# Kernel optimization log

Measured on AMD Instinct MI355X. Metric: run time of the kernel, lower is better.

Reference implementation:

```python
import jax, jax.numpy as jnp
import numpy as np
import math

D_MODEL, N_HEADS, SHARP = 1024, 16, 2.0
D_HEAD = D_MODEL // N_HEADS
B, S = 2, 2048


def setup_inputs() -> dict:
    key = jax.random.key(0)
    ks = jax.random.split(key, 12)
    s = 0.02
    d, h = D_MODEL, D_MODEL // 2
    return {
        'x': jax.random.normal(ks[0], (B, S, d), jnp.float32),
        'mask': jnp.ones((B, S), jnp.int32),
        'Wq': jax.random.normal(ks[1], (d, d), jnp.float32) * s,
        'bq': jnp.zeros((d,), jnp.float32),
        'Wk': jax.random.normal(ks[2], (d, d), jnp.float32) * s,
        'bk': jnp.zeros((d,), jnp.float32),
        'Wv': jax.random.normal(ks[3], (d, d), jnp.float32) * s,
        'bv': jnp.zeros((d,), jnp.float32),
        'Wo': jax.random.normal(ks[4], (d, d), jnp.float32) * s,
        'bo': jnp.zeros((d,), jnp.float32),
        'Wm1': jax.random.normal(ks[5], (h, d), jnp.float32) * s,
        'bm1': jnp.zeros((h,), jnp.float32),
        'Wm2': jax.random.normal(ks[6], (1, h), jnp.float32) * s,
        'bm2': jnp.zeros((1,), jnp.float32),
    }


def reference(x, mask, Wq, bq, Wk, bk, Wv, bv, Wo, bo, Wm1, bm1, Wm2, bm2):
    Bsz, Ssz, _ = x.shape
    lin = lambda t, W, b: jnp.einsum('bsd,ed->bse', t, W) + b  # torch Linear: x @ W.T + b
    split = lambda t: t.reshape(Bsz, Ssz, N_HEADS, D_HEAD).transpose(0, 2, 1, 3)  # [B,H,S,Dh]
    q, k, v = split(lin(x, Wq, bq)), split(lin(x, Wk, bk)), split(lin(x, Wv, bv))
    scores = jnp.einsum('bhqd,bhkd->bhqk', q, k) / math.sqrt(D_HEAD)  # [B,H,S,S]
    scores = jnp.where(mask[:, None, None, :] == 0, -jnp.inf, scores)
    # mechanism MLP: Linear -> GELU(exact) -> Linear -> [B,S]
    hmid = jax.nn.gelu(lin(x, Wm1, bm1), approximate=False)
    mech_logits = lin(hmid, Wm2, bm2).squeeze(-1)
    mech_strengths = jax.nn.softmax(mech_logits, axis=-1)  # [B,S]
    scores = scores + SHARP * mech_strengths[:, None, None, :]
    attn = jax.nn.softmax(scores, axis=-1)
    ctx = jnp.einsum('bhqk,bhkd->bhqd', attn, v)
    ctx = ctx.transpose(0, 2, 1, 3).reshape(Bsz, Ssz, D_MODEL)
    out = jnp.einsum('bsd,ed->bse', ctx, Wo) + bo
    return (out, mech_strengths)
```

## Files before the change

kernel.cpp:

```cpp
#include <hip/hip_runtime.h>
#include <hip/hip_fp16.h>
#include <math.h>

typedef _Float16 half4_t __attribute__((ext_vector_type(4)));
typedef _Float16 half8_t __attribute__((ext_vector_type(8)));
typedef float float4_t __attribute__((ext_vector_type(4)));

static constexpr int DMODEL = 1024;
static constexpr int SLEN   = 2048;
static constexpr int NHEADS = 16;
static constexpr int MTOT   = 4096;


__global__ __launch_bounds__(256) void pack_all_kernel(
    const float* __restrict__ x,
    const float* __restrict__ Wq, const float* __restrict__ Wk,
    const float* __restrict__ Wv, const float* __restrict__ Wo,
    const float* __restrict__ Wm1,
    _Float16* __restrict__ xP, _Float16* __restrict__ wqP,
    _Float16* __restrict__ wkP, _Float16* __restrict__ wvP,
    _Float16* __restrict__ woP, _Float16* __restrict__ wm1P) {
  int bx = blockIdx.x;
  const float* src; _Float16* dst; int lb;
  if (blockIdx.y == 0) {
    if (bx >= 2048) return;
    src = x; dst = xP; lb = bx;
  } else {
    if (bx < 512)       { src = Wq;  dst = wqP;  lb = bx; }
    else if (bx < 1024) { src = Wk;  dst = wkP;  lb = bx - 512; }
    else if (bx < 1536) { src = Wv;  dst = wvP;  lb = bx - 1024; }
    else if (bx < 2048) { src = Wo;  dst = woP;  lb = bx - 1536; }
    else                { src = Wm1; dst = wm1P; lb = bx - 2048; }
  }
  int c = lb * 256 + threadIdx.x;
  int lane = c & 63;
  int ks = (c >> 6) & 31;
  int rt = c >> 11;
  int row = 16 * rt + (lane & 15);
  int col = 32 * ks + 8 * (lane >> 4);
  const float* sp = src + (size_t)row * 1024 + col;
  float4_t v0 = *(const float4_t*)sp;
  float4_t v1 = *(const float4_t*)(sp + 4);
  half8_t h;
  h[0] = (_Float16)v0[0]; h[1] = (_Float16)v0[1];
  h[2] = (_Float16)v0[2]; h[3] = (_Float16)v0[3];
  h[4] = (_Float16)v1[0]; h[5] = (_Float16)v1[1];
  h[6] = (_Float16)v1[2]; h[7] = (_Float16)v1[3];
  *(half8_t*)(dst + (size_t)c * 8) = h;
}

__global__ __launch_bounds__(256, 2) void proj_kernel(
    const _Float16* __restrict__ xP,
    const _Float16* __restrict__ wqP, const _Float16* __restrict__ wkP,
    const _Float16* __restrict__ wvP, const _Float16* __restrict__ wm1P,
    const float* __restrict__ bq, const float* __restrict__ bk,
    const float* __restrict__ bv, const float* __restrict__ bm1,
    _Float16* __restrict__ Qh, _Float16* __restrict__ Kh,
    _Float16* __restrict__ Vh, _Float16* __restrict__ Hm) {
  int z = blockIdx.z;
  const _Float16* W; const float* bias; _Float16* out; int N; bool act = false;
  if (z == 0)      { W = wqP;  bias = bq;  out = Qh; N = 1024; }
  else if (z == 1) { W = wkP;  bias = bk;  out = Kh; N = 1024; }
  else if (z == 2) { W = wvP;  bias = bv;  out = Vh; N = 1024; }
  else             { W = wm1P; bias = bm1; out = Hm; N = 512; act = true; }
  int colB = blockIdx.y * 128;
  if (colB >= N) return;
  int wave = threadIdx.x >> 6, lane = threadIdx.x & 63;
  int lr = lane & 15, lg = lane >> 4;
  int row0 = blockIdx.x * 128 + (wave >> 1) * 64;
  int col0 = colB + (wave & 1) * 64;
  int rt0 = row0 >> 4, ct0 = col0 >> 4;
  float4_t acc[4][4];
#pragma unroll
  for (int i = 0; i < 4; i++)
#pragma unroll
    for (int j = 0; j < 4; j++) acc[i][j] = (float4_t){0.f, 0.f, 0.f, 0.f};
  for (int ks = 0; ks < 32; ks++) {
    half8_t af[4], bf[4];
#pragma unroll
    for (int i = 0; i < 4; i++)
      af[i] = *(const half8_t*)(xP + (((size_t)(rt0 + i) * 32 + ks) << 9) + (lane << 3));
#pragma unroll
    for (int j = 0; j < 4; j++)
      bf[j] = *(const half8_t*)(W + (((size_t)(ct0 + j) * 32 + ks) << 9) + (lane << 3));
#pragma unroll
    for (int i = 0; i < 4; i++)
#pragma unroll
      for (int j = 0; j < 4; j++)
        acc[i][j] = __builtin_amdgcn_mfma_f32_16x16x32_f16(af[i], bf[j], acc[i][j], 0, 0, 0);
  }
#pragma unroll
  for (int j = 0; j < 4; j++) {
    int col = col0 + 16 * j + lr;
    float bb = bias[col];
#pragma unroll
    for (int i = 0; i < 4; i++) {
#pragma unroll
      for (int r = 0; r < 4; r++) {
        int row = row0 + 16 * i + 4 * lg + r;
        float v = acc[i][j][r] + bb;
        if (act) v = 0.5f * v * (1.0f + erff(v * 0.70710678118f));
        out[(size_t)row * N + col] = (_Float16)v;
      }
    }
  }
}

__global__ __launch_bounds__(256, 2) void outproj_kernel(
    const _Float16* __restrict__ ctxh, const _Float16* __restrict__ woP,
    const float* __restrict__ bo, float* __restrict__ out) {
  int wave = threadIdx.x >> 6, lane = threadIdx.x & 63;
  int lr = lane & 15, lg = lane >> 4;
  int row0 = blockIdx.x * 128 + (wave >> 1) * 64;
  int col0 = blockIdx.y * 128 + (wave & 1) * 64;
  int ct0 = col0 >> 4;
  const _Float16* Ap = ctxh + (size_t)(row0 + lr) * 1024 + 8 * lg;
  float4_t acc[4][4];
#pragma unroll
  for (int i = 0; i < 4; i++)
#pragma unroll
    for (int j = 0; j < 4; j++) acc[i][j] = (float4_t){0.f, 0.f, 0.f, 0.f};
  for (int ks = 0; ks < 32; ks++) {
    half8_t af[4], bf[4];
#pragma unroll
    for (int i = 0; i < 4; i++)
      af[i] = *(const half8_t*)(Ap + (size_t)(16 * i) * 1024 + 32 * ks);
#pragma unroll
    for (int j = 0; j < 4; j++)
      bf[j] = *(const half8_t*)(woP + (((size_t)(ct0 + j) * 32 + ks) << 9) + (lane << 3));
#pragma unroll
    for (int i = 0; i < 4; i++)
#pragma unroll
      for (int j = 0; j < 4; j++)
        acc[i][j] = __builtin_amdgcn_mfma_f32_16x16x32_f16(af[i], bf[j], acc[i][j], 0, 0, 0);
  }
#pragma unroll
  for (int j = 0; j < 4; j++) {
    int col = col0 + 16 * j + lr;
    float bb = bo[col];
#pragma unroll
    for (int i = 0; i < 4; i++) {
#pragma unroll
      for (int r = 0; r < 4; r++) {
        int row = row0 + 16 * i + 4 * lg + r;
        out[(size_t)row * 1024 + col] = acc[i][j][r] + bb;
      }
    }
  }
}

__global__ __launch_bounds__(256) void mech_logits_kernel(
    const _Float16* __restrict__ Hm, const float* __restrict__ Wm2,
    const float* __restrict__ bm2, float* __restrict__ logits) {
  int wave = threadIdx.x >> 6, lane = threadIdx.x & 63;
  int row = blockIdx.x * 4 + wave;
  half8_t hv = *(const half8_t*)(Hm + (size_t)row * 512 + lane * 8);
  float4_t w0 = *(const float4_t*)(Wm2 + lane * 8);
  float4_t w1 = *(const float4_t*)(Wm2 + lane * 8 + 4);
  float s = 0.f;
#pragma unroll
  for (int j = 0; j < 4; j++) s += (float)hv[j] * w0[j];
#pragma unroll
  for (int j = 0; j < 4; j++) s += (float)hv[4 + j] * w1[j];
#pragma unroll
  for (int m = 32; m >= 1; m >>= 1) s += __shfl_xor(s, m, 64);
  if (lane == 0) logits[row] = s + bm2[0];
}

__global__ __launch_bounds__(256) void mech_softmax_kernel(
    const float* __restrict__ logits, float* __restrict__ mech_ws,
    float* __restrict__ mech_out) {
  int b = blockIdx.x;
  int t = threadIdx.x;
  int wave = t >> 6, lane = t & 63;
  __shared__ float redmax[4];
  __shared__ float redsum[4];
  const float4_t* L4 = (const float4_t*)(logits + (size_t)b * 2048);
  float4_t v0 = L4[2 * t], v1 = L4[2 * t + 1];
  float mx = fmaxf(fmaxf(fmaxf(v0[0], v0[1]), fmaxf(v0[2], v0[3])),
                   fmaxf(fmaxf(v1[0], v1[1]), fmaxf(v1[2], v1[3])));
#pragma unroll
  for (int m = 32; m >= 1; m >>= 1) mx = fmaxf(mx, __shfl_xor(mx, m, 64));
  if (lane == 0) redmax[wave] = mx;
  __syncthreads();
  mx = fmaxf(fmaxf(redmax[0], redmax[1]), fmaxf(redmax[2], redmax[3]));
  float e[8];
  float s = 0.f;
#pragma unroll
  for (int j = 0; j < 4; j++) { e[j] = __expf(v0[j] - mx); s += e[j]; }
#pragma unroll
  for (int j = 0; j < 4; j++) { e[4 + j] = __expf(v1[j] - mx); s += e[4 + j]; }
#pragma unroll
  for (int m = 32; m >= 1; m >>= 1) s += __shfl_xor(s, m, 64);
  if (lane == 0) redsum[wave] = s;
  __syncthreads();
  s = redsum[0] + redsum[1] + redsum[2] + redsum[3];
  float inv = 1.0f / s;
  size_t base = (size_t)b * 2048 + (size_t)t * 8;
#pragma unroll
  for (int j = 0; j < 8; j++) {
    float val = e[j] * inv;
    mech_ws[base + j] = val;
    mech_out[base + j] = val;
  }
}

__global__ __launch_bounds__(256) void kpack_kernel(const _Float16* __restrict__ Kh,
                                                    _Float16* __restrict__ KP) {
  int c = blockIdx.x * 256 + threadIdx.x;
  int lane = c & 63;
  int c2 = (c >> 6) & 1;
  int kt = (c >> 7) & 127;
  int bh = c >> 14;
  int b = bh >> 4, h = bh & 15;
  int lr = lane & 15, lg = lane >> 4;
  const _Float16* sp = Kh + (size_t)(b * 2048 + 16 * kt + lr) * 1024 + h * 64 + 32 * c2 + 8 * lg;
  *(half8_t*)(KP + (size_t)c * 8) = *(const half8_t*)sp;
}

__global__ __launch_bounds__(256) void vpack_kernel(const _Float16* __restrict__ Vh,
                                                    _Float16* __restrict__ VP) {
  int bh = blockIdx.y;
  int b = bh >> 4, h = bh & 15;
  int k0 = blockIdx.x * 64;
  __shared__ _Float16 tile[64][68];
  int t = threadIdx.x;
#pragma unroll
  for (int rep = 0; rep < 16; rep++) {
    int idx = rep * 256 + t;
    int k = idx >> 6, d = idx & 63;
    tile[d][k] = Vh[(size_t)(b * 2048 + k0 + k) * 1024 + h * 64 + d];
  }
  __syncthreads();
  _Float16* outb = VP + (((size_t)bh * 128 + (k0 >> 4)) << 10);
#pragma unroll
  for (int rep = 0; rep < 4; rep++) {
    int o4 = rep * 256 + t;
    int lane = o4 & 63;
    int dd = (o4 >> 6) & 3;
    int ktp = o4 >> 8;
    int d = 16 * dd + (lane & 15);
    int k = 16 * ktp + 4 * (lane >> 4);
    half4_t v = *(const half4_t*)&tile[d][k];
    *(half4_t*)(outb + (size_t)o4 * 4) = v;
  }
}

__global__ __launch_bounds__(256, 2) void attn_kernel(
    const _Float16* __restrict__ Qh, const _Float16* __restrict__ KP,
    const _Float16* __restrict__ VP, const float* __restrict__ mech,
    const int* __restrict__ mask, _Float16* __restrict__ ctxh) {
  __shared__ float bias_s[2048];
  int bh = blockIdx.y;
  int b = bh >> 4, h = bh & 15;
  for (int i = threadIdx.x; i < 2048; i += 256)
    bias_s[i] = 2.0f * mech[(size_t)b * 2048 + i] +
                (mask[(size_t)b * 2048 + i] != 0 ? 0.0f : -1e30f);
  __syncthreads();
  int wave = threadIdx.x >> 6, lane = threadIdx.x & 63;
  int lr = lane & 15, lg = lane >> 4;
  int q0 = blockIdx.x * 128 + wave * 32;

  const _Float16* Qbase = Qh + (size_t)(b * 2048 + q0 + lr) * 1024 + h * 64 + 8 * lg;
  half8_t qf[2][2];
  qf[0][0] = *(const half8_t*)(Qbase);
  qf[0][1] = *(const half8_t*)(Qbase + 32);
  qf[1][0] = *(const half8_t*)(Qbase + (size_t)16 * 1024);
  qf[1][1] = *(const half8_t*)(Qbase + (size_t)16 * 1024 + 32);
  const _Float16* KPbh = KP + ((size_t)bh << 17);
  const _Float16* VPbh = VP + ((size_t)bh << 17);

  float m0 = -1e30f, m1 = -1e30f;
  float l0 = 0.0f, l1 = 0.0f;
  float4_t cacc[2][4];
#pragma unroll
  for (int g = 0; g < 2; g++)
#pragma unroll
    for (int dd = 0; dd < 4; dd++) cacc[g][dd] = (float4_t){0.f, 0.f, 0.f, 0.f};

  for (int k0 = 0; k0 < 2048; k0 += 64) {
    int kt0 = k0 >> 4;
    half8_t kf[4][2];
#pragma unroll
    for (int t = 0; t < 4; t++) {
      kf[t][0] = *(const half8_t*)(KPbh + (((size_t)(kt0 + t) * 2 + 0) << 9) + (lane << 3));
      kf[t][1] = *(const half8_t*)(KPbh + (((size_t)(kt0 + t) * 2 + 1) << 9) + (lane << 3));
    }
    half4_t vf[4][4];
#pragma unroll
    for (int dd = 0; dd < 4; dd++)
#pragma unroll
      for (int t = 0; t < 4; t++)
        vf[dd][t] = *(const half4_t*)(VPbh + (((size_t)(kt0 + t) * 4 + dd) << 8) + (lane << 2));
    float4_t bias4[4];
#pragma unroll
    for (int t = 0; t < 4; t++)
      bias4[t] = *(const float4_t*)&bias_s[k0 + 16 * t + 4 * lg];
    float4_t s0[4], s1[4];
#pragma unroll
    for (int t = 0; t < 4; t++) {
      float4_t z = (float4_t){0.f, 0.f, 0.f, 0.f};
      z = __builtin_amdgcn_mfma_f32_16x16x32_f16(kf[t][0], qf[0][0], z, 0, 0, 0);
      z = __builtin_amdgcn_mfma_f32_16x16x32_f16(kf[t][1], qf[0][1], z, 0, 0, 0);
      s0[t] = z;
      float4_t w = (float4_t){0.f, 0.f, 0.f, 0.f};
      w = __builtin_amdgcn_mfma_f32_16x16x32_f16(kf[t][0], qf[1][0], w, 0, 0, 0);
      w = __builtin_amdgcn_mfma_f32_16x16x32_f16(kf[t][1], qf[1][1], w, 0, 0, 0);
      s1[t] = w;
    }
#pragma unroll
    for (int t = 0; t < 4; t++)
#pragma unroll
      for (int r = 0; r < 4; r++) {
        s0[t][r] = s0[t][r] * 0.125f + bias4[t][r];
        s1[t][r] = s1[t][r] * 0.125f + bias4[t][r];
      }
    float tm0 = s0[0][0], tm1 = s1[0][0];
#pragma unroll
    for (int t = 0; t < 4; t++)
#pragma unroll
      for (int r = 0; r < 4; r++) {
        tm0 = fmaxf(tm0, s0[t][r]);
        tm1 = fmaxf(tm1, s1[t][r]);
      }
    tm0 = fmaxf(tm0, __shfl_xor(tm0, 16, 64));
    tm0 = fmaxf(tm0, __shfl_xor(tm0, 32, 64));
    tm1 = fmaxf(tm1, __shfl_xor(tm1, 16, 64));
    tm1 = fmaxf(tm1, __shfl_xor(tm1, 32, 64));
    if (__any((tm0 > m0 + 8.0f) || (tm1 > m1 + 8.0f))) {
      float mn0 = fmaxf(m0, tm0), mn1 = fmaxf(m1, tm1);
      float a0 = __expf(m0 - mn0), a1 = __expf(m1 - mn1);
      l0 *= a0; l1 *= a1;
      m0 = mn0; m1 = mn1;
      int rbase = 4 * lg;
#pragma unroll
      for (int r = 0; r < 4; r++) {
        float b0 = __shfl(a0, rbase + r, 64);
        float b1 = __shfl(a1, rbase + r, 64);
#pragma unroll
        for (int dd = 0; dd < 4; dd++) {
          cacc[0][dd][r] *= b0;
          cacc[1][dd][r] *= b1;
        }
      }
    }
    half4_t pa0[4], pa1[4];
#pragma unroll
    for (int t = 0; t < 4; t++) {
#pragma unroll
      for (int r = 0; r < 4; r++) {
        float p0 = __expf(s0[t][r] - m0);
        float p1 = __expf(s1[t][r] - m1);
        l0 += p0; l1 += p1;
        pa0[t][r] = (_Float16)p0;
        pa1[t][r] = (_Float16)p1;
      }
    }
#pragma unroll
    for (int dd = 0; dd < 4; dd++)
#pragma unroll
      for (int t = 0; t < 4; t++) {
        cacc[0][dd] = __builtin_amdgcn_mfma_f32_16x16x16f16(pa0[t], vf[dd][t], cacc[0][dd], 0, 0, 0);
        cacc[1][dd] = __builtin_amdgcn_mfma_f32_16x16x16f16(pa1[t], vf[dd][t], cacc[1][dd], 0, 0, 0);
      }
  }
  l0 += __shfl_xor(l0, 16, 64);
  l0 += __shfl_xor(l0, 32, 64);
  l1 += __shfl_xor(l1, 16, 64);
  l1 += __shfl_xor(l1, 32, 64);
  float li0 = 1.0f / l0, li1 = 1.0f / l1;
  int rbase = 4 * lg;
#pragma unroll
  for (int r = 0; r < 4; r++) {
    float i0 = __shfl(li0, rbase + r, 64);
    float i1 = __shfl(li1, rbase + r, 64);
#pragma unroll
    for (int dd = 0; dd < 4; dd++) {
      size_t idx0 = (size_t)(b * 2048 + q0 + rbase + r) * 1024 + h * 64 + 16 * dd + lr;
      size_t idx1 = (size_t)(b * 2048 + q0 + 16 + rbase + r) * 1024 + h * 64 + 16 * dd + lr;
      ctxh[idx0] = (_Float16)(cacc[0][dd][r] * i0);
      ctxh[idx1] = (_Float16)(cacc[1][dd][r] * i1);
    }
  }
}

extern "C" void kernel_launch(void* const* d_in, const int* in_sizes, int n_in,
                              void* d_out, int out_size, void* d_ws, size_t ws_size,
                              hipStream_t stream) {
  const float* x    = (const float*)d_in[0];
  const int*   mask = (const int*)d_in[1];
  const float* Wq   = (const float*)d_in[2];
  const float* bq   = (const float*)d_in[3];
  const float* Wk   = (const float*)d_in[4];
  const float* bk   = (const float*)d_in[5];
  const float* Wv   = (const float*)d_in[6];
  const float* bv   = (const float*)d_in[7];
  const float* Wo   = (const float*)d_in[8];
  const float* bo   = (const float*)d_in[9];
  const float* Wm1  = (const float*)d_in[10];
  const float* bm1  = (const float*)d_in[11];
  const float* Wm2  = (const float*)d_in[12];
  const float* bm2  = (const float*)d_in[13];
  float* outp = (float*)d_out;
  float* mech_out = outp + (size_t)MTOT * DMODEL;

  char* ws = (char*)d_ws;
  _Float16* xP   = (_Float16*)(ws + 0);
  _Float16* wqP  = (_Float16*)(ws + 8388608);
  _Float16* wkP  = (_Float16*)(ws + 10485760);
  _Float16* wvP  = (_Float16*)(ws + 12582912);
  _Float16* woP  = (_Float16*)(ws + 14680064);
  _Float16* wm1P = (_Float16*)(ws + 16777216);
  _Float16* Qh   = (_Float16*)(ws + 17825792);
  _Float16* Kh   = (_Float16*)(ws + 26214400);
  _Float16* Vh   = (_Float16*)(ws + 34603008);
  _Float16* VP   = (_Float16*)(ws + 42991616);
  _Float16* ctxh = (_Float16*)(ws + 51380224);
  _Float16* Hm   = (_Float16*)(ws + 59768832);
  float* logits  = (float*)(ws + 63963136);
  float* mech_ws = (float*)(ws + 63979520);
  _Float16* KPp  = xP;

  hipLaunchKernelGGL(pack_all_kernel, dim3(2304, 2), dim3(256), 0, stream,
                     x, Wq, Wk, Wv, Wo, Wm1, xP, wqP, wkP, wvP, woP, wm1P);

  hipLaunchKernelGGL(proj_kernel, dim3(32, 8, 4), dim3(256), 0, stream,
                     xP, wqP, wkP, wvP, wm1P, bq, bk, bv, bm1, Qh, Kh, Vh, Hm);

  hipLaunchKernelGGL(mech_logits_kernel, dim3(1024), dim3(256), 0, stream,
                     Hm, Wm2, bm2, logits);
  hipLaunchKernelGGL(mech_softmax_kernel, dim3(2), dim3(256), 0, stream,
                     logits, mech_ws, mech_out);

  hipLaunchKernelGGL(kpack_kernel, dim3(2048), dim3(256), 0, stream, Kh, KPp);
  hipLaunchKernelGGL(vpack_kernel, dim3(32, 32), dim3(256), 0, stream, Vh, VP);

  hipLaunchKernelGGL(attn_kernel, dim3(16, 32), dim3(256), 0, stream,
                     Qh, KPp, VP, mech_ws, mask, ctxh);

  hipLaunchKernelGGL(outproj_kernel, dim3(32, 8), dim3(256), 0, stream,
                     ctxh, woP, bo, outp);
}
```

Before: 274.8 us.

## Double-buffer GEMM fragment loads and emit attention context in MFMA-packed layout

The projection and output-projection GEMM loops now prefetch the next k-step's A/B fragments into a second register set while MFMAs run on the current set, hiding global load latency. The attention kernel stages its normalized output through shared memory and writes it in the tile-packed fragment layout, so the output projection can read A fragments as contiguous 16-byte lane chunks instead of strided rows. This costs extra registers for the double buffers and an extra LDS round trip in the attention epilogue.

Result: faster. 263.4 us (-4.1%).

```diff
diff --git a/kernel.cpp b/kernel.cpp
--- a/kernel.cpp
+++ b/kernel.cpp
@@ -70,25 +70,56 @@
   int row0 = blockIdx.x * 128 + (wave >> 1) * 64;
   int col0 = colB + (wave & 1) * 64;
   int rt0 = row0 >> 4, ct0 = col0 >> 4;
+  const _Float16* Ab = xP + (((size_t)rt0 * 32) << 9) + (lane << 3);
+  const _Float16* Bb = W  + (((size_t)ct0 * 32) << 9) + (lane << 3);
   float4_t acc[4][4];
 #pragma unroll
   for (int i = 0; i < 4; i++)
 #pragma unroll
     for (int j = 0; j < 4; j++) acc[i][j] = (float4_t){0.f, 0.f, 0.f, 0.f};
-  for (int ks = 0; ks < 32; ks++) {
-    half8_t af[4], bf[4];
+  half8_t aP[4], bP[4], aN[4], bN[4];
+#pragma unroll
+  for (int i = 0; i < 4; i++) {
+    aP[i] = *(const half8_t*)(Ab + ((size_t)(i * 32) << 9));
+    bP[i] = *(const half8_t*)(Bb + ((size_t)(i * 32) << 9));
+  }
+  for (int ks = 0; ks < 30; ks += 2) {
+#pragma unroll
+    for (int i = 0; i < 4; i++) {
+      aN[i] = *(const half8_t*)(Ab + ((size_t)(i * 32 + ks + 1) << 9));
+      bN[i] = *(const half8_t*)(Bb + ((size_t)(i * 32 + ks + 1) << 9));
+    }
 #pragma unroll
     for (int i = 0; i < 4; i++)
-      af[i] = *(const half8_t*)(xP + (((size_t)(rt0 + i) * 32 + ks) << 9) + (lane << 3));
+#pragma unroll
+      for (int j = 0; j < 4; j++)
+        acc[i][j] = __builtin_amdgcn_mfma_f32_16x16x32_f16(aP[i], bP[j], acc[i][j], 0, 0, 0);
+#pragma unroll
+    for (int i = 0; i < 4; i++) {
+      aP[i] = *(const half8_t*)(Ab + ((size_t)(i * 32 + ks + 2) << 9));
+      bP[i] = *(const half8_t*)(Bb + ((size_t)(i * 32 + ks + 2) << 9));
+    }
+#pragma unroll
+    for (int i = 0; i < 4; i++)
+#pragma unroll
+      for (int j = 0; j < 4; j++)
+        acc[i][j] = __builtin_amdgcn_mfma_f32_16x16x32_f16(aN[i], bN[j], acc[i][j], 0, 0, 0);
+  }
+#pragma unroll
+  for (int i = 0; i < 4; i++) {
+    aN[i] = *(const half8_t*)(Ab + ((size_t)(i * 32 + 31) << 9));
+    bN[i] = *(const half8_t*)(Bb + ((size_t)(i * 32 + 31) << 9));
+  }
+#pragma unroll
+  for (int i = 0; i < 4; i++)
 #pragma unroll
     for (int j = 0; j < 4; j++)
-      bf[j] = *(const half8_t*)(W + (((size_t)(ct0 + j) * 32 + ks) << 9) + (lane << 3));
-#pragma unroll
-    for (int i = 0; i < 4; i++)
-#pragma unroll
-      for (int j = 0; j < 4; j++)
-        acc[i][j] = __builtin_amdgcn_mfma_f32_16x16x32_f16(af[i], bf[j], acc[i][j], 0, 0, 0);
-  }
+      acc[i][j] = __builtin_amdgcn_mfma_f32_16x16x32_f16(aP[i], bP[j], acc[i][j], 0, 0, 0);
+#pragma unroll
+  for (int i = 0; i < 4; i++)
+#pragma unroll
+    for (int j = 0; j < 4; j++)
+      acc[i][j] = __builtin_amdgcn_mfma_f32_16x16x32_f16(aN[i], bN[j], acc[i][j], 0, 0, 0);
 #pragma unroll
   for (int j = 0; j < 4; j++) {
     int col = col0 + 16 * j + lr;
@@ -107,33 +138,63 @@
 }
 
 __global__ __launch_bounds__(256, 2) void outproj_kernel(
-    const _Float16* __restrict__ ctxh, const _Float16* __restrict__ woP,
+    const _Float16* __restrict__ ctxP, const _Float16* __restrict__ woP,
     const float* __restrict__ bo, float* __restrict__ out) {
   int wave = threadIdx.x >> 6, lane = threadIdx.x & 63;
   int lr = lane & 15, lg = lane >> 4;
   int row0 = blockIdx.x * 128 + (wave >> 1) * 64;
   int col0 = blockIdx.y * 128 + (wave & 1) * 64;
-  int ct0 = col0 >> 4;
-  const _Float16* Ap = ctxh + (size_t)(row0 + lr) * 1024 + 8 * lg;
+  int rt0 = row0 >> 4, ct0 = col0 >> 4;
+  const _Float16* Ab = ctxP + (((size_t)rt0 * 32) << 9) + (lane << 3);
+  const _Float16* Bb = woP  + (((size_t)ct0 * 32) << 9) + (lane << 3);
   float4_t acc[4][4];
 #pragma unroll
   for (int i = 0; i < 4; i++)
 #pragma unroll
     for (int j = 0; j < 4; j++) acc[i][j] = (float4_t){0.f, 0.f, 0.f, 0.f};
-  for (int ks = 0; ks < 32; ks++) {
-    half8_t af[4], bf[4];
+  half8_t aP[4], bP[4], aN[4], bN[4];
+#pragma unroll
+  for (int i = 0; i < 4; i++) {
+    aP[i] = *(const half8_t*)(Ab + ((size_t)(i * 32) << 9));
+    bP[i] = *(const half8_t*)(Bb + ((size_t)(i * 32) << 9));
+  }
+  for (int ks = 0; ks < 30; ks += 2) {
+#pragma unroll
+    for (int i = 0; i < 4; i++) {
+      aN[i] = *(const half8_t*)(Ab + ((size_t)(i * 32 + ks + 1) << 9));
+      bN[i] = *(const half8_t*)(Bb + ((size_t)(i * 32 + ks + 1) << 9));
+    }
 #pragma unroll
     for (int i = 0; i < 4; i++)
-      af[i] = *(const half8_t*)(Ap + (size_t)(16 * i) * 1024 + 32 * ks);
+#pragma unroll
+      for (int j = 0; j < 4; j++)
+        acc[i][j] = __builtin_amdgcn_mfma_f32_16x16x32_f16(aP[i], bP[j], acc[i][j], 0, 0, 0);
+#pragma unroll
+    for (int i = 0; i < 4; i++) {
+      aP[i] = *(const half8_t*)(Ab + ((size_t)(i * 32 + ks + 2) << 9));
+      bP[i] = *(const half8_t*)(Bb + ((size_t)(i * 32 + ks + 2) << 9));
+    }
+#pragma unroll
+    for (int i = 0; i < 4; i++)
+#pragma unroll
+      for (int j = 0; j < 4; j++)
+        acc[i][j] = __builtin_amdgcn_mfma_f32_16x16x32_f16(aN[i], bN[j], acc[i][j], 0, 0, 0);
+  }
+#pragma unroll
+  for (int i = 0; i < 4; i++) {
+    aN[i] = *(const half8_t*)(Ab + ((size_t)(i * 32 + 31) << 9));
+    bN[i] = *(const half8_t*)(Bb + ((size_t)(i * 32 + 31) << 9));
+  }
+#pragma unroll
+  for (int i = 0; i < 4; i++)
 #pragma unroll
     for (int j = 0; j < 4; j++)
-      bf[j] = *(const half8_t*)(woP + (((size_t)(ct0 + j) * 32 + ks) << 9) + (lane << 3));
-#pragma unroll
-    for (int i = 0; i < 4; i++)
-#pragma unroll
-      for (int j = 0; j < 4; j++)
-        acc[i][j] = __builtin_amdgcn_mfma_f32_16x16x32_f16(af[i], bf[j], acc[i][j], 0, 0, 0);
-  }
+      acc[i][j] = __builtin_amdgcn_mfma_f32_16x16x32_f16(aP[i], bP[j], acc[i][j], 0, 0, 0);
+#pragma unroll
+  for (int i = 0; i < 4; i++)
+#pragma unroll
+    for (int j = 0; j < 4; j++)
+      acc[i][j] = __builtin_amdgcn_mfma_f32_16x16x32_f16(aN[i], bN[j], acc[i][j], 0, 0, 0);
 #pragma unroll
   for (int j = 0; j < 4; j++) {
     int col = col0 + 16 * j + lr;
@@ -249,8 +310,9 @@
 __global__ __launch_bounds__(256, 2) void attn_kernel(
     const _Float16* __restrict__ Qh, const _Float16* __restrict__ KP,
     const _Float16* __restrict__ VP, const float* __restrict__ mech,
-    const int* __restrict__ mask, _Float16* __restrict__ ctxh) {
+    const int* __restrict__ mask, _Float16* __restrict__ ctxP) {
   __shared__ float bias_s[2048];
+  __shared__ _Float16 ep[4][4][512];
   int bh = blockIdx.y;
   int b = bh >> 4, h = bh & 15;
   for (int i = threadIdx.x; i < 2048; i += 256)
@@ -370,17 +432,27 @@
   l1 += __shfl_xor(l1, 32, 64);
   float li0 = 1.0f / l0, li1 = 1.0f / l1;
   int rbase = 4 * lg;
+  float inv0[4], inv1[4];
 #pragma unroll
   for (int r = 0; r < 4; r++) {
-    float i0 = __shfl(li0, rbase + r, 64);
-    float i1 = __shfl(li1, rbase + r, 64);
-#pragma unroll
-    for (int dd = 0; dd < 4; dd++) {
-      size_t idx0 = (size_t)(b * 2048 + q0 + rbase + r) * 1024 + h * 64 + 16 * dd + lr;
-      size_t idx1 = (size_t)(b * 2048 + q0 + 16 + rbase + r) * 1024 + h * 64 + 16 * dd + lr;
-      ctxh[idx0] = (_Float16)(cacc[0][dd][r] * i0);
-      ctxh[idx1] = (_Float16)(cacc[1][dd][r] * i1);
-    }
+    inv0[r] = __shfl(li0, rbase + r, 64);
+    inv1[r] = __shfl(li1, rbase + r, 64);
+  }
+#pragma unroll
+  for (int dd = 0; dd < 4; dd++) {
+    int lanep = ((dd & 1) * 2 + (lr >> 3)) * 16 + rbase;
+#pragma unroll
+    for (int r = 0; r < 4; r++) {
+      ep[wave][0 + (dd >> 1)][(lanep + r) * 8 + (lr & 7)] = (_Float16)(cacc[0][dd][r] * inv0[r]);
+      ep[wave][2 + (dd >> 1)][(lanep + r) * 8 + (lr & 7)] = (_Float16)(cacc[1][dd][r] * inv1[r]);
+    }
+  }
+  int rtbase = (b * 2048 + q0) >> 4;
+#pragma unroll
+  for (int c = 0; c < 4; c++) {
+    half8_t v = *(const half8_t*)&ep[wave][c][lane * 8];
+    size_t chunkid = (size_t)(rtbase + (c >> 1)) * 32 + (2 * h + (c & 1));
+    *(half8_t*)(ctxP + (chunkid << 9) + (lane << 3)) = v;
   }
 }
 
@@ -415,7 +487,7 @@
   _Float16* Kh   = (_Float16*)(ws + 26214400);
   _Float16* Vh   = (_Float16*)(ws + 34603008);
   _Float16* VP   = (_Float16*)(ws + 42991616);
-  _Float16* ctxh = (_Float16*)(ws + 51380224);
+  _Float16* ctxP = (_Float16*)(ws + 51380224);
   _Float16* Hm   = (_Float16*)(ws + 59768832);
   float* logits  = (float*)(ws + 63963136);
   float* mech_ws = (float*)(ws + 63979520);
@@ -436,8 +508,8 @@
   hipLaunchKernelGGL(vpack_kernel, dim3(32, 32), dim3(256), 0, stream, Vh, VP);
 
   hipLaunchKernelGGL(attn_kernel, dim3(16, 32), dim3(256), 0, stream,
-                     Qh, KPp, VP, mech_ws, mask, ctxh);
+                     Qh, KPp, VP, mech_ws, mask, ctxP);
 
   hipLaunchKernelGGL(outproj_kernel, dim3(32, 8), dim3(256), 0, stream,
-                     ctxh, woP, bo, outp);
-}
+                     ctxP, woP, bo, outp);
+}
```
